# Kernel tuning notes

Measured on AMD Instinct MI355X. Metric: run time of the kernel, lower is better.

Reference implementation:

```python
import jax, jax.numpy as jnp
import numpy as np

N, D1, D2, BW, B = 8, 1024, 1024, 3, 1024
D = D1 * D2
RES_DENOS = [3.0, 5.0, 17.0, 257.0, 65537.0]  # [2^2-1, 2^2+1, 2^4+1, 2^8+1, 2^16+1]
SPLIT_TEMP = 0.01


def ste_floor(x):
    # forward: floor, backward: identity (matches custom round autograd.Function)
    return x + jax.lax.stop_gradient(jnp.floor(x) - x)


def quantize_weights(U, thres_mean):
    beta, alpha = jnp.max(U), jnp.min(U)
    s = (beta - alpha) / RES_DENOS[0]
    vals_sum = s * ste_floor(U / s)  # level 0
    col = jnp.arange(D)[None, :]
    for idx in range(1, BW):
        s = s / RES_DENOS[idx]
        res_err = U - vals_sum                                   # [N, D]
        order = jnp.argsort(res_err, axis=0)                     # [N, D] int
        sorted_err = jnp.take_along_axis(res_err, order, axis=0) # [N, D]
        delta = sorted_err[1:] - sorted_err[:-1]                 # [N-1, D]
        delta = delta / jnp.max(delta)
        # differentiable split points, one per gap between sorted rows
        sp = jax.nn.sigmoid((jnp.mean(delta, axis=1) - jax.nn.sigmoid(thres_mean)[0]) / SPLIT_TEMP)  # [N-1]
        b = jnp.round(sp)                                        # hard 0/1 boundary (zero grad, like torch branch)
        gid = jnp.concatenate([jnp.zeros((1,), sp.dtype), jnp.cumsum(b)]).astype(jnp.int32)  # [N] group id per row
        counts = jax.ops.segment_sum(jnp.ones((N,), U.dtype), gid, num_segments=N)           # [N]
        sums = jax.ops.segment_sum(sorted_err, gid, num_segments=N)                          # [N, D]
        means = sums / jnp.maximum(counts, 1.0)[:, None]
        # grad_ factor: sp at boundary rows, (1-sp) at interior rows, 1 for the last row
        factors = jnp.where(b == 1.0, sp, 1.0 - sp)              # [N-1], in (0,1)
        logf = jnp.concatenate([jnp.log(factors), jnp.zeros((1,), sp.dtype)])  # [N]
        grad_g = jnp.exp(jax.ops.segment_sum(logf, gid, num_segments=N))       # [N] per-group product
        t = grad_g[gid][:, None] * means[gid]                    # [N, D] group value broadcast to member rows
        # scatter back through the sort permutation (== one-hot transfer matmul)
        grouped = jnp.zeros_like(U).at[order, col].set(t)
        vals_sum = vals_sum + s * ste_floor(grouped / s)
    return vals_sum


def setup_inputs() -> dict:
    key = jax.random.key(0)
    kx, ku = jax.random.split(key)
    x = jax.random.normal(kx, (B, N, D1), dtype=jnp.float32)
    # kaiming_normal_ on (N, D): std = sqrt(2 / fan_in) with fan_in = D
    U = jax.random.normal(ku, (N, D), dtype=jnp.float32) * np.sqrt(2.0 / D).astype(np.float32)
    thres_mean = jnp.array([-0.405], dtype=jnp.float32)
    return {"x": x, "U": U, "thres_mean": thres_mean}


def reference(x, U, thres_mean):
    w = quantize_weights(U, thres_mean).reshape(N, D1, D2)
    return jnp.einsum('bnd,ndl->bnl', x, w)
```

## Files before the change

kernel.cpp:

```cpp
#include <hip/hip_runtime.h>
#include <hip/hip_bf16.h>
#include <stdint.h>

#define DD (1 << 20)

typedef float v4f __attribute__((ext_vector_type(4)));
typedef __bf16 bf16x8 __attribute__((ext_vector_type(8)));

struct Scalars {
  float s;
  int   uniform;
  float coef[8];
  float cnti[8];
  int   isend[8];
};

struct Partial {
  double g[7];
  double mx;
};

static __device__ __forceinline__ unsigned short f2bf(float v) {
  unsigned u = __float_as_uint(v);
  u += 0x7fffu + ((u >> 16) & 1u);
  return (unsigned short)(u >> 16);
}

#define CE2(a, b)                                                        \
  { float ra = r[a], rb = r[b]; int oa = ord[a], ob = ord[b];            \
    bool sw = (ra > rb) || (ra == rb && oa > ob);                        \
    r[a] = sw ? rb : ra; r[b] = sw ? ra : rb;                            \
    ord[a] = sw ? ob : oa; ord[b] = sw ? oa : ob; }

#define SORTNET8                                                          \
  CE2(0,1) CE2(2,3) CE2(4,5) CE2(6,7)                                     \
  CE2(0,2) CE2(1,3) CE2(4,6) CE2(5,7)                                     \
  CE2(1,2) CE2(5,6)                                                       \
  CE2(0,4) CE2(1,5) CE2(2,6) CE2(3,7)                                     \
  CE2(2,4) CE2(3,5)                                                       \
  CE2(1,2) CE2(3,4) CE2(5,6)

#define CEV(a, b) { float ra = q[a], rb = q[b]; q[a] = fminf(ra, rb); q[b] = fmaxf(ra, rb); }
#define SORTNET8V                                                         \
  CEV(0,1) CEV(2,3) CEV(4,5) CEV(6,7)                                     \
  CEV(0,2) CEV(1,3) CEV(4,6) CEV(5,7)                                     \
  CEV(1,2) CEV(5,6)                                                       \
  CEV(0,4) CEV(1,5) CEV(2,6) CEV(3,7)                                     \
  CEV(2,4) CEV(3,5)                                                       \
  CEV(1,2) CEV(3,4) CEV(5,6)

static __device__ __forceinline__ void stats_block_reduce(float dl[7], float mx,
                                                          Partial* __restrict__ po) {
#pragma unroll
  for (int off = 32; off; off >>= 1) {
#pragma unroll
    for (int g = 0; g < 7; ++g) dl[g] += __shfl_down(dl[g], off, 64);
    mx = fmaxf(mx, __shfl_down(mx, off, 64));
  }
  __shared__ double wsum[4][7];
  __shared__ float wmax[4];
  int lane = threadIdx.x & 63, wv = threadIdx.x >> 6;
  if (lane == 0) {
#pragma unroll
    for (int g = 0; g < 7; ++g) wsum[wv][g] = (double)dl[g];
    wmax[wv] = mx;
  }
  __syncthreads();
  if (threadIdx.x == 0) {
#pragma unroll
    for (int g = 0; g < 7; ++g)
      po->g[g] = wsum[0][g] + wsum[1][g] + wsum[2][g] + wsum[3][g];
    po->mx = (double)fmaxf(fmaxf(wmax[0], wmax[1]), fmaxf(wmax[2], wmax[3]));
  }
}

static __device__ __forceinline__ float compute_s0(const float2* __restrict__ mmpart) {
  __shared__ float2 wmm[4];
  __shared__ float sS0;
  int t = threadIdx.x;
  float mn = 3.4e38f, mxv = -3.4e38f;
#pragma unroll
  for (int j = 0; j < 4; ++j) {
    float2 p = mmpart[j * 256 + t];
    mn = fminf(mn, p.x); mxv = fmaxf(mxv, p.y);
  }
#pragma unroll
  for (int off = 32; off; off >>= 1) {
    mn = fminf(mn, __shfl_down(mn, off, 64));
    mxv = fmaxf(mxv, __shfl_down(mxv, off, 64));
  }
  int lane = t & 63, wv = t >> 6;
  if (lane == 0) wmm[wv] = make_float2(mn, mxv);
  __syncthreads();
  if (t == 0) {
    for (int i = 1; i < 4; ++i) { mn = fminf(mn, wmm[i].x); mxv = fmaxf(mxv, wmm[i].y); }
    sS0 = (mxv - mn) / 3.0f;
  }
  __syncthreads();
  return sS0;
}

static __device__ __forceinline__ void reduce_partials(const Partial* __restrict__ part,
                                                       double g[7], double& mx) {
  __shared__ double sg[4][8];
  int t = threadIdx.x;
  __syncthreads();
#pragma unroll
  for (int i = 0; i < 7; ++i) g[i] = 0.0;
  mx = 0.0;
#pragma unroll
  for (int j = 0; j < 4; ++j) {
    const Partial& p = part[j * 256 + t];
#pragma unroll
    for (int i = 0; i < 7; ++i) g[i] += p.g[i];
    mx = fmax(mx, p.mx);
  }
#pragma unroll
  for (int off = 32; off; off >>= 1) {
#pragma unroll
    for (int i = 0; i < 7; ++i) g[i] += __shfl_down(g[i], off, 64);
    mx = fmax(mx, __shfl_down(mx, off, 64));
  }
  int lane = t & 63, wv = t >> 6;
  if (lane == 0) {
#pragma unroll
    for (int i = 0; i < 7; ++i) sg[wv][i] = g[i];
    sg[wv][7] = mx;
  }
  __syncthreads();
  if (t == 0) {
#pragma unroll
    for (int i = 0; i < 7; ++i) g[i] = sg[0][i] + sg[1][i] + sg[2][i] + sg[3][i];
    mx = fmax(fmax(sg[0][7], sg[1][7]), fmax(sg[2][7], sg[3][7]));
  }
}

static __device__ void make_scalars(const double g[7], double mx, float s_prev, float deno,
                                    float thres0, Scalars* sc, bool* sat) {
  float s = s_prev / deno;
  sc->s = s;
  float md = (float)mx;
  float sigT = 1.f / (1.f + expf(-thres0));
  float sp[7], bb[7];
  float zmax = -1e30f;
  for (int gg = 0; gg < 7; ++gg) {
    float mean = (float)(g[gg] / ((double)DD * (double)md));
    float z = (mean - sigT) / 0.01f;
    zmax = fmaxf(zmax, z);
    sp[gg] = 1.f / (1.f + expf(-z));
    bb[gg] = rintf(sp[gg]);
  }
  int gid[8]; gid[0] = 0;
  for (int i = 1; i < 8; ++i) gid[i] = gid[i - 1] + (int)bb[i - 1];
  float counts[8] = {0, 0, 0, 0, 0, 0, 0, 0};
  for (int i = 0; i < 8; ++i) counts[gid[i]] += 1.f;
  float lsum[8] = {0, 0, 0, 0, 0, 0, 0, 0};
  for (int i = 0; i < 7; ++i) {
    float f = (bb[i] == 1.f) ? sp[i] : (1.f - sp[i]);
    lsum[gid[i]] += logf(f);
  }
  float gradg[8];
  for (int gg = 0; gg < 8; ++gg) gradg[gg] = expf(lsum[gg]);
  for (int i = 0; i < 8; ++i) {
    sc->coef[i] = gradg[gid[i]];
    sc->cnti[i] = fmaxf(counts[gid[i]], 1.f);
    sc->isend[i] = (i == 7) || (gid[i + 1] != gid[i]);
  }
  int uni = (gid[7] == 0) ? 1 : 0;
  sc->uniform = uni;
  *sat = (uni && zmax < -21.0f);
}

static __device__ __forceinline__ void update_core(const float u[8], const float vo[8],
                                                   const Scalars* __restrict__ sc,
                                                   float vnew[8]) {
  float s = sc->s;
  float coef[8], cnti[8]; int isend[8];
#pragma unroll
  for (int i = 0; i < 8; ++i) { coef[i] = sc->coef[i]; cnti[i] = sc->cnti[i]; isend[i] = sc->isend[i]; }
  float r[8]; int ord[8];
#pragma unroll
  for (int n = 0; n < 8; ++n) { r[n] = u[n] - vo[n]; ord[n] = n; }
  SORTNET8
  float endsum[8]; float a = 0.f;
#pragma unroll
  for (int i = 0; i < 8; ++i) { a += r[i]; endsum[i] = a; if (isend[i]) a = 0.f; }
  float t[8]; float gsv = 0.f;
#pragma unroll
  for (int i = 7; i >= 0; --i) {
    if (isend[i]) gsv = endsum[i];
    t[i] = coef[i] * (gsv / cnti[i]);
  }
#pragma unroll
  for (int n = 0; n < 8; ++n) {
    float tv = 0.f;
#pragma unroll
    for (int i = 0; i < 8; ++i) tv = (ord[i] == n) ? t[i] : tv;
    vnew[n] = vo[n] + s * floorf(tv / s);
  }
}

static __device__ __forceinline__ float uniform_delta(const float u[8], const float vo[8],
                                                      float coef0, float cnt0, float s) {
  float q[8];
#pragma unroll
  for (int n = 0; n < 8; ++n) q[n] = u[n] - vo[n];
  SORTNET8V
  float a = 0.f;
#pragma unroll
  for (int i = 0; i < 8; ++i) a += q[i];
  float t = coef0 * (a / cnt0);
  return s * floorf(t / s);
}

static __device__ __forceinline__ void apply_update(const float u[8], const float vo[8],
                                                    const Scalars* __restrict__ sc,
                                                    float vnew[8]) {
  if (sc->uniform) {
    float c = uniform_delta(u, vo, sc->coef[0], sc->cnti[0], sc->s);
#pragma unroll
    for (int n = 0; n < 8; ++n) vnew[n] = vo[n] + c;
  } else {
    update_core(u, vo, sc, vnew);
  }
}

__global__ __launch_bounds__(256)
void k1_minmax_xpack(const float4* __restrict__ U4, float2* __restrict__ mmpart,
                     const float* __restrict__ x, unsigned short* __restrict__ xT) {
  int tid = threadIdx.x;
  if (blockIdx.x < 1024) {
    int bid = blockIdx.x;
    float mn = 3.4e38f, mx = -3.4e38f;
#pragma unroll
    for (int j = 0; j < 8; ++j) {
      float4 v = U4[(size_t)(bid * 8 + j) * 256 + tid];
      mn = fminf(mn, fminf(fminf(v.x, v.y), fminf(v.z, v.w)));
      mx = fmaxf(mx, fmaxf(fmaxf(v.x, v.y), fmaxf(v.z, v.w)));
    }
#pragma unroll
    for (int off = 32; off; off >>= 1) {
      mn = fminf(mn, __shfl_down(mn, off, 64));
      mx = fmaxf(mx, __shfl_down(mx, off, 64));
    }
    __shared__ float2 w4[4];
    if ((tid & 63) == 0) w4[tid >> 6] = make_float2(mn, mx);
    __syncthreads();
    if (tid == 0) {
      for (int i = 1; i < 4; ++i) { mn = fminf(mn, w4[i].x); mx = fmaxf(mx, w4[i].y); }
      mmpart[bid] = make_float2(mn, mx);
    }
  } else {
    int bid2 = blockIdx.x - 1024;
#pragma unroll
    for (int j = 0; j < 4; ++j) {
      int i = j * (2048 * 256) + bid2 * 256 + tid;
      int kq = i & 255;
      int b  = (i >> 8) & 1023;
      int n  = i >> 18;
      float4 v = *(const float4*)(x + ((size_t)(b * 8 + n) << 10) + (kq << 2));
      ushort4 o = make_ushort4(f2bf(v.x), f2bf(v.y), f2bf(v.z), f2bf(v.w));
      *(ushort4*)(xT + (((size_t)(n << 10 | b)) << 10) + (kq << 2)) = o;
    }
  }
}

__global__ __launch_bounds__(256)
void k2_stats0(const float* __restrict__ U, const float2* __restrict__ mmpart,
               Partial* __restrict__ part) {
  float s0 = compute_s0(mmpart);
  int t = threadIdx.x;
  size_t d0 = (size_t)blockIdx.x * 1024 + t * 4;
  float4 u4[8];
#pragma unroll
  for (int n = 0; n < 8; ++n) u4[n] = *(const float4*)(U + ((size_t)n << 20) + d0);
  float dl[7] = {0, 0, 0, 0, 0, 0, 0};
  float mxv = 0.f;
#pragma unroll
  for (int j = 0; j < 4; ++j) {
    float q[8];
#pragma unroll
    for (int n = 0; n < 8; ++n) {
      float u = ((const float*)&u4[n])[j];
      q[n] = u - s0 * floorf(u / s0);
    }
    SORTNET8V
#pragma unroll
    for (int g = 0; g < 7; ++g) { float dd = q[g + 1] - q[g]; dl[g] += dd; mxv = fmaxf(mxv, dd); }
  }
  stats_block_reduce(dl, mxv, &part[blockIdx.x]);
}

__global__ __launch_bounds__(256)
void k3a_stats1(const float* __restrict__ U, const float2* __restrict__ mmpart,
                const Partial* __restrict__ part, Partial* __restrict__ part2,
                const float* __restrict__ thres) {
  __shared__ Scalars ssc1;
  __shared__ int ssat;
  float s0 = compute_s0(mmpart);
  double g[7]; double mx;
  reduce_partials(part, g, mx);
  if (threadIdx.x == 0) {
    bool sat;
    make_scalars(g, mx, s0, 5.0f, thres[0], &ssc1, &sat);
    ssat = sat ? 1 : 0;
  }
  __syncthreads();
  if (ssat) return;

  int t = threadIdx.x;
  size_t d0 = (size_t)blockIdx.x * 1024 + t * 4;
  float4 u4[8];
#pragma unroll
  for (int n = 0; n < 8; ++n) u4[n] = *(const float4*)(U + ((size_t)n << 20) + d0);
  float dl[7] = {0, 0, 0, 0, 0, 0, 0};
  float mxv = 0.f;
#pragma unroll
  for (int j = 0; j < 4; ++j) {
    float u[8], v0[8], v1[8];
#pragma unroll
    for (int n = 0; n < 8; ++n) {
      u[n] = ((const float*)&u4[n])[j];
      v0[n] = s0 * floorf(u[n] / s0);
    }
    apply_update(u, v0, &ssc1, v1);
    float q[8];
#pragma unroll
    for (int n = 0; n < 8; ++n) q[n] = u[n] - v1[n];
    SORTNET8V
#pragma unroll
    for (int gg = 0; gg < 7; ++gg) { float dd = q[gg + 1] - q[gg]; dl[gg] += dd; mxv = fmaxf(mxv, dd); }
  }
  stats_block_reduce(dl, mxv, &part2[blockIdx.x]);
}

__global__ __launch_bounds__(256)
void k3b_final(const float* __restrict__ U, const float2* __restrict__ mmpart,
               const Partial* __restrict__ part, const Partial* __restrict__ part2,
               const float* __restrict__ thres, unsigned short* __restrict__ wT) {
  __shared__ Scalars ssc1, ssc2;
  __shared__ int ssat;
  __shared__ unsigned short stile[8][32][34];
  int t = threadIdx.x;
  float s0 = compute_s0(mmpart);
  {
    double g[7]; double mx;
    reduce_partials(part, g, mx);
    if (t == 0) {
      bool sat;
      make_scalars(g, mx, s0, 5.0f, thres[0], &ssc1, &sat);
      ssat = sat ? 1 : 0;
    }
  }
  __syncthreads();
  if (!ssat) {
    double g[7]; double mx;
    reduce_partials(part2, g, mx);
    if (t == 0) {
      bool sat2;
      make_scalars(g, mx, ssc1.s, 17.0f, thres[0], &ssc2, &sat2);
    }
  } else if (t == 0) {
    ssc2.s = ssc1.s / 17.0f;
    ssc2.uniform = 1;
#pragma unroll
    for (int i = 0; i < 8; ++i) {
      ssc2.coef[i] = 1.0f;
      ssc2.cnti[i] = 8.0f;
      ssc2.isend[i] = (i == 7) ? 1 : 0;
    }
  }
  __syncthreads();

  int k0 = (blockIdx.x >> 5) * 32;
  int l0 = (blockIdx.x & 31) * 32;
  int kk = t >> 3;
  int lq = t & 7;
  int d0 = (k0 + kk) * 1024 + l0 + lq * 4;
  float4 u4[8];
#pragma unroll
  for (int n = 0; n < 8; ++n) u4[n] = *(const float4*)(U + ((size_t)n << 20) + d0);
#pragma unroll
  for (int j = 0; j < 4; ++j) {
    float u[8], v0[8], v1[8], v2[8];
#pragma unroll
    for (int n = 0; n < 8; ++n) {
      u[n] = ((const float*)&u4[n])[j];
      v0[n] = s0 * floorf(u[n] / s0);
    }
    apply_update(u, v0, &ssc1, v1);
    apply_update(u, v1, &ssc2, v2);
#pragma unroll
    for (int n = 0; n < 8; ++n) stile[n][kk][lq * 4 + j] = f2bf(v2[n]);
  }
  __syncthreads();
  int ll = t >> 3, kq = t & 7;
#pragma unroll
  for (int n = 0; n < 8; ++n) {
    ushort4 o;
    o.x = stile[n][kq * 4 + 0][ll];
    o.y = stile[n][kq * 4 + 1][ll];
    o.z = stile[n][kq * 4 + 2][ll];
    o.w = stile[n][kq * 4 + 3][ll];
    *(ushort4*)(wT + ((size_t)n << 20) + (size_t)(l0 + ll) * 1024 + k0 + kq * 4) = o;
  }
}

__global__ __launch_bounds__(256, 2)
void k_gemm(const unsigned short* __restrict__ xT, const unsigned short* __restrict__ wT,
            float* __restrict__ out) {
  __shared__ bf16x8 sA[1024];
  __shared__ bf16x8 sB[1024];
  const int n  = blockIdx.x;
  const int m0 = blockIdx.y * 128;
  const int l0 = blockIdx.z * 128;
  const int tid = threadIdx.x;
  const int lane = tid & 63;
  const int wv = tid >> 6;
  const int wm = (wv & 1) * 64;
  const int wl = (wv >> 1) * 64;
  const unsigned short* A  = xT + ((size_t)n << 20);
  const unsigned short* Bt = wT + ((size_t)n << 20);

  v4f acc[4][4] = {};
  const int quad = lane >> 4;
  const int r16 = lane & 15;

  for (int kt = 0; kt < 1024; kt += 64) {
#pragma unroll
    for (int rr = 0; rr < 4; ++rr) {
      int cb = rr * 4 + wv;
      int c = cb * 64 + lane;
      int row = c >> 3;
      int gc = (c & 7) ^ (row & 7);
      const unsigned short* ga = A  + (size_t)(m0 + row) * 1024 + kt + gc * 8;
      const unsigned short* gb = Bt + (size_t)(l0 + row) * 1024 + kt + gc * 8;
      __builtin_amdgcn_global_load_lds((const __attribute__((address_space(1))) void*)ga,
                                       (__attribute__((address_space(3))) void*)&sA[cb * 64],
                                       16, 0, 0);
      __builtin_amdgcn_global_load_lds((const __attribute__((address_space(1))) void*)gb,
                                       (__attribute__((address_space(3))) void*)&sB[cb * 64],
                                       16, 0, 0);
    }
    asm volatile("s_waitcnt vmcnt(0)" ::: "memory");
    __syncthreads();

#pragma unroll
    for (int ks = 0; ks < 2; ++ks) {
      bf16x8 af[4], bfr[4];
#pragma unroll
      for (int tt = 0; tt < 4; ++tt) {
        int arow = wm + tt * 16 + r16;
        af[tt] = sA[arow * 8 + ((ks * 4 + quad) ^ (arow & 7))];
        int brow = wl + tt * 16 + r16;
        bfr[tt] = sB[brow * 8 + ((ks * 4 + quad) ^ (brow & 7))];
      }
#pragma unroll
      for (int tm = 0; tm < 4; ++tm)
#pragma unroll
        for (int tn = 0; tn < 4; ++tn)
          acc[tm][tn] = __builtin_amdgcn_mfma_f32_16x16x32_bf16(af[tm], bfr[tn], acc[tm][tn], 0, 0, 0);
    }
    __syncthreads();
  }

#pragma unroll
  for (int tm = 0; tm < 4; ++tm)
#pragma unroll
    for (int tn = 0; tn < 4; ++tn)
#pragma unroll
      for (int rr = 0; rr < 4; ++rr) {
        int row = m0 + wm + tm * 16 + quad * 4 + rr;
        int col = l0 + wl + tn * 16 + r16;
        out[(size_t)(row * 8 + n) * 1024 + col] = acc[tm][tn][rr];
      }
}

extern "C" void kernel_launch(void* const* d_in, const int* in_sizes, int n_in,
                              void* d_out, int out_size, void* d_ws, size_t ws_size,
                              hipStream_t stream) {
  const float* x = (const float*)d_in[0];
  const float* U = (const float*)d_in[1];
  const float* thres = (const float*)d_in[2];
  float* out = (float*)d_out;

  char* w = (char*)d_ws;
  float2* mmpart = (float2*)w;
  Partial* part  = (Partial*)(w + 8192);
  Partial* part2 = (Partial*)(w + 8192 + 65536);
  unsigned short* xT = (unsigned short*)(w + (1 << 20));
  unsigned short* wT = xT + ((size_t)8 << 20);

  k1_minmax_xpack<<<3072, 256, 0, stream>>>((const float4*)U, mmpart, x, xT);
  k2_stats0<<<1024, 256, 0, stream>>>(U, mmpart, part);
  k3a_stats1<<<1024, 256, 0, stream>>>(U, mmpart, part, part2, thres);
  k3b_final<<<1024, 256, 0, stream>>>(U, mmpart, part, part2, thres, wT);
  k_gemm<<<dim3(8, 8, 8), 256, 0, stream>>>(xT, wT, out);
}
```

Baseline: 168.1 us.

## Triple-buffer GEMM LDS loads with 256x128 tiles and 512-thread blocks

Reworks the batched GEMM into a 3-stage software pipeline. Global-to-LDS async loads for tile k+2 are issued while tile k is computed, and partial vmcnt waits replace the full drain. The block tile grows to 256x128 with 8 waves, and MFMA sections are bracketed with s_setprio to favour matrix issue. The aim is to hide global memory latency and improve reuse, at the cost of 144 KB of LDS per block, which limits occupancy to one block per CU despite the launch bounds of 2, and halves the grid to 256 blocks.

New measurement: 171.1 us. No clear change (+1.8%).

```diff
diff --git a/kernel.cpp b/kernel.cpp
--- a/kernel.cpp
+++ b/kernel.cpp
@@ -406,19 +406,19 @@
   }
 }
 
-__global__ __launch_bounds__(256, 2)
+__global__ __launch_bounds__(512, 2)
 void k_gemm(const unsigned short* __restrict__ xT, const unsigned short* __restrict__ wT,
             float* __restrict__ out) {
-  __shared__ bf16x8 sA[1024];
-  __shared__ bf16x8 sB[1024];
+  __shared__ bf16x8 sA[3][2048];
+  __shared__ bf16x8 sB[3][1024];
   const int n  = blockIdx.x;
-  const int m0 = blockIdx.y * 128;
+  const int m0 = blockIdx.y * 256;
   const int l0 = blockIdx.z * 128;
   const int tid = threadIdx.x;
   const int lane = tid & 63;
   const int wv = tid >> 6;
-  const int wm = (wv & 1) * 64;
-  const int wl = (wv >> 1) * 64;
+  const int wm = (wv & 3) * 64;
+  const int wl = (wv >> 2) * 64;
   const unsigned short* A  = xT + ((size_t)n << 20);
   const unsigned short* Bt = wT + ((size_t)n << 20);
 
@@ -426,43 +426,75 @@
   const int quad = lane >> 4;
   const int r16 = lane & 15;
 
-  for (int kt = 0; kt < 1024; kt += 64) {
-#pragma unroll
-    for (int rr = 0; rr < 4; ++rr) {
-      int cb = rr * 4 + wv;
-      int c = cb * 64 + lane;
-      int row = c >> 3;
-      int gc = (c & 7) ^ (row & 7);
-      const unsigned short* ga = A  + (size_t)(m0 + row) * 1024 + kt + gc * 8;
-      const unsigned short* gb = Bt + (size_t)(l0 + row) * 1024 + kt + gc * 8;
-      __builtin_amdgcn_global_load_lds((const __attribute__((address_space(1))) void*)ga,
-                                       (__attribute__((address_space(3))) void*)&sA[cb * 64],
-                                       16, 0, 0);
-      __builtin_amdgcn_global_load_lds((const __attribute__((address_space(1))) void*)gb,
-                                       (__attribute__((address_space(3))) void*)&sB[cb * 64],
-                                       16, 0, 0);
-    }
-    asm volatile("s_waitcnt vmcnt(0)" ::: "memory");
-    __syncthreads();
-
-#pragma unroll
-    for (int ks = 0; ks < 2; ++ks) {
-      bf16x8 af[4], bfr[4];
-#pragma unroll
-      for (int tt = 0; tt < 4; ++tt) {
-        int arow = wm + tt * 16 + r16;
-        af[tt] = sA[arow * 8 + ((ks * 4 + quad) ^ (arow & 7))];
-        int brow = wl + tt * 16 + r16;
-        bfr[tt] = sB[brow * 8 + ((ks * 4 + quad) ^ (brow & 7))];
-      }
-#pragma unroll
-      for (int tm = 0; tm < 4; ++tm)
-#pragma unroll
-        for (int tn = 0; tn < 4; ++tn)
-          acc[tm][tn] = __builtin_amdgcn_mfma_f32_16x16x32_bf16(af[tm], bfr[tn], acc[tm][tn], 0, 0, 0);
-    }
-    __syncthreads();
-  }
+#define GSTAGE(buf, kt)                                                                   \
+  {                                                                                       \
+    _Pragma("unroll")                                                                     \
+    for (int rr = 0; rr < 4; ++rr) {                                                      \
+      int c = rr * 512 + tid;                                                             \
+      int row = c >> 3;                                                                   \
+      int gc = (c & 7) ^ (row & 7);                                                       \
+      const unsigned short* ga = A + (size_t)(m0 + row) * 1024 + (kt) + gc * 8;           \
+      __builtin_amdgcn_global_load_lds((const __attribute__((address_space(1))) void*)ga, \
+          (__attribute__((address_space(3))) void*)&sA[buf][rr * 512 + wv * 64], 16, 0, 0); \
+    }                                                                                     \
+    _Pragma("unroll")                                                                     \
+    for (int rr = 0; rr < 2; ++rr) {                                                      \
+      int c = rr * 512 + tid;                                                             \
+      int row = c >> 3;                                                                   \
+      int gc = (c & 7) ^ (row & 7);                                                       \
+      const unsigned short* gb = Bt + (size_t)(l0 + row) * 1024 + (kt) + gc * 8;          \
+      __builtin_amdgcn_global_load_lds((const __attribute__((address_space(1))) void*)gb, \
+          (__attribute__((address_space(3))) void*)&sB[buf][rr * 512 + wv * 64], 16, 0, 0); \
+    }                                                                                     \
+  }
+
+#define GCOMPUTE(buf)                                                                     \
+  {                                                                                       \
+    _Pragma("unroll")                                                                     \
+    for (int ks = 0; ks < 2; ++ks) {                                                      \
+      bf16x8 af[4], bfr[4];                                                               \
+      _Pragma("unroll")                                                                   \
+      for (int tt = 0; tt < 4; ++tt) {                                                    \
+        int arow = wm + tt * 16 + r16;                                                    \
+        af[tt] = sA[buf][arow * 8 + ((ks * 4 + quad) ^ (arow & 7))];                      \
+        int brow = wl + tt * 16 + r16;                                                    \
+        bfr[tt] = sB[buf][brow * 8 + ((ks * 4 + quad) ^ (brow & 7))];                     \
+      }                                                                                   \
+      __builtin_amdgcn_s_setprio(1);                                                      \
+      _Pragma("unroll")                                                                   \
+      for (int tm = 0; tm < 4; ++tm)                                                      \
+        _Pragma("unroll")                                                                 \
+        for (int tn = 0; tn < 4; ++tn)                                                    \
+          acc[tm][tn] = __builtin_amdgcn_mfma_f32_16x16x32_bf16(af[tm], bfr[tn],          \
+                                                                acc[tm][tn], 0, 0, 0);   \
+      __builtin_amdgcn_s_setprio(0);                                                      \
+    }                                                                                     \
+  }
+
+  GSTAGE(0, 0)
+  GSTAGE(1, 64)
+  asm volatile("s_waitcnt vmcnt(6)" ::: "memory");
+  __builtin_amdgcn_s_barrier();
+  asm volatile("" ::: "memory");
+
+  for (int t = 0; t < 14; ++t) {
+    const int buf = t % 3;
+    const int nbuf = (t + 2) % 3;
+    GSTAGE(nbuf, (t + 2) * 64)
+    GCOMPUTE(buf)
+    asm volatile("s_waitcnt lgkmcnt(0)" ::: "memory");
+    asm volatile("s_waitcnt vmcnt(6)" ::: "memory");
+    __builtin_amdgcn_s_barrier();
+    asm volatile("" ::: "memory");
+  }
+  GCOMPUTE(2)
+  asm volatile("s_waitcnt lgkmcnt(0)" ::: "memory");
+  asm volatile("s_waitcnt vmcnt(0)" ::: "memory");
+  __builtin_amdgcn_s_barrier();
+  asm volatile("" ::: "memory");
+  GCOMPUTE(0)
+#undef GSTAGE
+#undef GCOMPUTE
 
 #pragma unroll
   for (int tm = 0; tm < 4; ++tm)
@@ -495,5 +527,5 @@
   k2_stats0<<<1024, 256, 0, stream>>>(U, mmpart, part);
   k3a_stats1<<<1024, 256, 0, stream>>>(U, mmpart, part, part2, thres);
   k3b_final<<<1024, 256, 0, stream>>>(U, mmpart, part, part2, thres, wT);
-  k_gemm<<<dim3(8, 8, 8), 256, 0, stream>>>(xT, wT, out);
-}
+  k_gemm<<<dim3(8, 4, 8), 512, 0, stream>>>(xT, wT, out);
+}
```
